# Optimization experiments

Measured on AMD Instinct MI355X. Metric: run time of the kernel, lower is better.

Reference implementation:

```python
import jax, jax.numpy as jnp
import numpy as np

N_NODES = 50000
N_EDGES = 1600000
N_GRAPHS = 512
HEADS = 4
HEAD_DIM = 32
LAYERS = 3
NEG_SLOPE = 0.2


def setup_inputs() -> dict:
    key = jax.random.key(0)
    ks = jax.random.split(key, 7)
    x = jax.random.normal(ks[0], (N_NODES, 128), dtype=jnp.float32)
    Ws = jax.random.normal(ks[1], (LAYERS, 128, 128), dtype=jnp.float32) * 0.1
    att_src = jax.random.normal(ks[2], (LAYERS, HEADS, HEAD_DIM), dtype=jnp.float32) * 0.1
    att_dst = jax.random.normal(ks[3], (LAYERS, HEADS, HEAD_DIM), dtype=jnp.float32) * 0.1
    biases = jnp.zeros((LAYERS, 128), dtype=jnp.float32)
    edge_index = jax.random.randint(ks[4], (2, N_EDGES), 0, N_NODES, dtype=jnp.int64)
    batch = jnp.sort(jax.random.randint(ks[5], (N_NODES,), 0, N_GRAPHS, dtype=jnp.int64))
    return {"x": x, "Ws": Ws, "att_src": att_src, "att_dst": att_dst,
            "biases": biases, "edge_index": edge_index, "batch": batch}


def _gat_layer(x, W, a_s, a_d, b, src, dst, n):
    # linear transform -> per-head features [N, H, C]
    h = (x @ W).reshape(n, HEADS, HEAD_DIM)
    # per-node attention halves [N, H]
    alpha_src = jnp.einsum('nhc,hc->nh', h, a_s)
    alpha_dst = jnp.einsum('nhc,hc->nh', h, a_d)
    # edge logits [E, H]
    e = jax.nn.leaky_relu(alpha_src[src] + alpha_dst[dst], NEG_SLOPE)
    # segment softmax over incoming edges of each destination node
    m = jax.ops.segment_max(e, dst, num_segments=n)
    w = jnp.exp(e - m[dst])
    denom = jax.ops.segment_sum(w, dst, num_segments=n)
    alpha = w / (denom[dst] + 1e-16)
    # weighted scatter-add of source features [E, H, C] -> [N, H, C]
    msg = h[src] * alpha[:, :, None]
    out = jax.ops.segment_sum(msg, dst, num_segments=n)
    return out.reshape(n, HEADS * HEAD_DIM) + b


def reference(x, Ws, att_src, att_dst, biases, edge_index, batch):
    n = x.shape[0]
    # PyG GATConv adds self-loops by default
    loops = jnp.arange(n, dtype=edge_index.dtype)
    src = jnp.concatenate([edge_index[0], loops])
    dst = jnp.concatenate([edge_index[1], loops])
    for l in range(LAYERS):
        x = jax.nn.elu(_gat_layer(x, Ws[l], att_src[l], att_dst[l], biases[l], src, dst, n))
        # dropout is identity in eval mode
    # global mean pool over graphs
    sums = jax.ops.segment_sum(x, batch, num_segments=N_GRAPHS)
    cnt = jax.ops.segment_sum(jnp.ones((n,), x.dtype), batch, num_segments=N_GRAPHS)
    return sums / jnp.maximum(cnt, 1.0)[:, None]
```

## Files before the change

kernel.cpp:

```cpp
#include <hip/hip_runtime.h>
#include <hip/hip_fp16.h>
#include <math.h>

#define HEADS 4
#define HDIM 32
#define FD 128
#define NEG 0.2f
#define BCAP 4608
#define CH 8192
#define CHW 128

typedef _Float16 f16x8 __attribute__((ext_vector_type(8)));
typedef float f32x4 __attribute__((ext_vector_type(4)));

__device__ __forceinline__ float lrelu(float x) { return fmaxf(x, NEG * x); }

__global__ __launch_bounds__(256) void k_prep(const float* __restrict__ x,
                                              __half* __restrict__ o, long nF,
                                              const float* __restrict__ W,
                                              const float* __restrict__ att_s,
                                              const float* __restrict__ att_d,
                                              _Float16* __restrict__ W16T,
                                              float* __restrict__ va_s,
                                              float* __restrict__ va_d,
                                              int* __restrict__ bcnt, int nbuck,
                                              int ncvt) {
    int b = blockIdx.x;
    if (b < ncvt) {
        long i = ((long)b * 256 + threadIdx.x) * 4;
        if (i < nF) {
            float4 v = *(const float4*)&x[i];
            *(__half2*)&o[i] = __floats2half2_rn(v.x, v.y);
            *(__half2*)&o[i + 2] = __floats2half2_rn(v.z, v.w);
        }
        return;
    }
    if (b == ncvt + 3) {
        for (int i = threadIdx.x; i < nbuck; i += 256) bcnt[i] = 0;
        return;
    }
    int l = b - ncvt;
    const float* Wl = W + (long)l * FD * FD;
    _Float16* ow = W16T + (long)l * FD * FD;
    for (int i = threadIdx.x; i < FD * FD; i += 256) {
        int k = i >> 7, n = i & 127;
        ow[n * FD + k] = (_Float16)Wl[i];
    }
    const float* as_l = att_s + l * HEADS * HDIM;
    const float* ad_l = att_d + l * HEADS * HDIM;
    for (int idx = threadIdx.x; idx < HEADS * FD; idx += 256) {
        int hd = idx >> 7, k = idx & 127;
        float ss = 0.f, dd = 0.f;
        for (int c = 0; c < HDIM; ++c) {
            float w = Wl[k * FD + hd * HDIM + c];
            ss += w * as_l[hd * HDIM + c];
            dd += w * ad_l[hd * HDIM + c];
        }
        va_s[(long)l * HEADS * FD + idx] = ss;
        va_d[(long)l * HEADS * FD + idx] = dd;
    }
}

__global__ __launch_bounds__(256) void k_gemm_mfma(const __half* __restrict__ x16,
                                                   const _Float16* __restrict__ W16T,
                                                   __half* __restrict__ h, int N) {
    __shared__ _Float16 wl[FD * FD];
    int t = threadIdx.x;
    for (int i = t * 8; i < FD * FD; i += 2048)
        *(f16x8*)&wl[i] = *(const f16x8*)&W16T[i];

    int w = t >> 6, lane = t & 63;
    int m = lane & 15, quad = lane >> 4;
    int row0 = blockIdx.x * 128 + w * 32;

    f16x8 a[2][4];
    f16x8 zf = {};
#pragma unroll
    for (int rt = 0; rt < 2; ++rt) {
        int gr = row0 + rt * 16 + m;
#pragma unroll
        for (int kc = 0; kc < 4; ++kc)
            a[rt][kc] = (gr < N) ? *(const f16x8*)&x16[(long)gr * FD + kc * 32 + quad * 8] : zf;
    }
    f32x4 acc[2][8];
#pragma unroll
    for (int rt = 0; rt < 2; ++rt)
#pragma unroll
        for (int c = 0; c < 8; ++c) acc[rt][c] = (f32x4){0.f, 0.f, 0.f, 0.f};

    __syncthreads();
#pragma unroll
    for (int c = 0; c < 8; ++c) {
        int nb = c * 16 + m;
#pragma unroll
        for (int kc = 0; kc < 4; ++kc) {
            f16x8 b = *(f16x8*)&wl[nb * FD + kc * 32 + quad * 8];
            acc[0][c] = __builtin_amdgcn_mfma_f32_16x16x32_f16(a[0][kc], b, acc[0][c], 0, 0, 0);
            acc[1][c] = __builtin_amdgcn_mfma_f32_16x16x32_f16(a[1][kc], b, acc[1][c], 0, 0, 0);
        }
    }
#pragma unroll
    for (int rt = 0; rt < 2; ++rt) {
        int rbase = row0 + rt * 16 + quad * 4;
#pragma unroll
        for (int c = 0; c < 8; ++c) {
            int col = c * 16 + m;
#pragma unroll
            for (int i = 0; i < 4; ++i) {
                int gr = rbase + i;
                if (gr < N) h[(long)gr * FD + col] = __float2half(acc[rt][c][i]);
            }
        }
    }
}

__global__ __launch_bounds__(256) void k_alpha(const __half* __restrict__ h,
                                               const float* __restrict__ a_s,
                                               const float* __restrict__ a_d,
                                               float* __restrict__ as_o,
                                               float* __restrict__ ad_o, int N) {
    int t = threadIdx.x;
    int n = blockIdx.x * 16 + (t >> 4);
    if (n >= N) return;
    int c16 = t & 15, gh = c16 >> 2, cb = c16 * 8;
    int c32 = (c16 & 3) * 8;
    float4 raw = *(const float4*)&h[(long)n * FD + cb];
    const __half* hh = (const __half*)&raw;
    float vs = 0.f, vd = 0.f;
#pragma unroll
    for (int i = 0; i < 8; ++i) {
        float hv = __half2float(hh[i]);
        vs += hv * a_s[gh * HDIM + c32 + i];
        vd += hv * a_d[gh * HDIM + c32 + i];
    }
    vs += __shfl_xor(vs, 1); vs += __shfl_xor(vs, 2);
    vd += __shfl_xor(vd, 1); vd += __shfl_xor(vd, 2);
    if ((c16 & 3) == 0) {
        as_o[n * HEADS + gh] = vs;
        ad_o[n * HEADS + gh] = vd;
    }
}

__global__ __launch_bounds__(1024) void k_bin(const int* __restrict__ ei, int NE,
                                              int nbuck,
                                              int* __restrict__ bcnt,
                                              int* __restrict__ binned) {
    __shared__ int hist[512];
    __shared__ int gbase[512];
    int t = threadIdx.x;
    int c0 = blockIdx.x * CH;
    if (t < 512) hist[t] = 0;
    __syncthreads();
    int sub[8], val[8], loff[8];
#pragma unroll
    for (int k = 0; k < 8; ++k) {
        int idx = c0 + k * 1024 + t;
        sub[k] = -1;
        if (idx < NE) {
            int s = ei[idx], d = ei[NE + idx];
            sub[k] = d >> 7;
            val[k] = s | ((d & 127) << 16);
            loff[k] = atomicAdd(&hist[sub[k]], 1);
        }
    }
    __syncthreads();
    if (t < 512 && t < nbuck && hist[t] > 0)
        gbase[t] = atomicAdd(&bcnt[t], hist[t]);
    __syncthreads();
#pragma unroll
    for (int k = 0; k < 8; ++k) {
        if (sub[k] >= 0) {
            int p = gbase[sub[k]] + loff[k];
            if (p < BCAP) binned[(long)sub[k] * BCAP + p] = val[k];
        }
    }
}

__global__ __launch_bounds__(1024) void k_scan_sub(const int* __restrict__ bcnt,
                                                   int* __restrict__ bbase, int n,
                                                   int* __restrict__ rowstart, int N, int NE,
                                                   float* __restrict__ cnt, int G,
                                                   float* __restrict__ outz) {
    __shared__ int sm[1024];
    int t = threadIdx.x;
    int c0 = t * 4;
    int v0 = (c0 < n) ? bcnt[c0] : 0;
    int v1 = (c0 + 1 < n) ? bcnt[c0 + 1] : 0;
    int v2 = (c0 + 2 < n) ? bcnt[c0 + 2] : 0;
    int v3 = (c0 + 3 < n) ? bcnt[c0 + 3] : 0;
    int tot = v0 + v1 + v2 + v3;
    sm[t] = tot;
    if (t < G) cnt[t] = 0.f;
    __syncthreads();
    for (int off = 1; off < 1024; off <<= 1) {
        int u = (t >= off) ? sm[t - off] : 0;
        __syncthreads();
        sm[t] += u;
        __syncthreads();
    }
    int base = sm[t] - tot;
    if (c0 < n) bbase[c0] = base;
    if (c0 + 1 < n) bbase[c0 + 1] = base + v0;
    if (c0 + 2 < n) bbase[c0 + 2] = base + v0 + v1;
    if (c0 + 3 < n) bbase[c0 + 3] = base + v0 + v1 + v2;
    if (t == 1023) {
        bbase[n] = sm[1023];
        rowstart[N] = NE;
    }
    long tot_out = (long)G * FD;
    for (long i = t * 4; i < tot_out; i += 4096)
        *(float4*)&outz[i] = (float4){0.f, 0.f, 0.f, 0.f};
}

__global__ __launch_bounds__(256) void k_bucket_csr(const int* __restrict__ binned,
                                                    const int* __restrict__ bcnt,
                                                    const int* __restrict__ bbase,
                                                    int* __restrict__ csr_src,
                                                    int* __restrict__ rowstart, int N) {
    int b = blockIdx.x;
    int t = threadIdx.x;
    __shared__ int ldeg[128], lofs[128], lcur[128];
    __shared__ int lcsr[BCAP];
    if (t < 128) ldeg[t] = 0;
    __syncthreads();
    int cnt = bcnt[b];
    if (cnt > BCAP) cnt = BCAP;
    int base = bbase[b];
    const int* reg = binned + (long)b * BCAP;
    for (int i = t; i < cnt; i += 256)
        atomicAdd(&ldeg[reg[i] >> 16], 1);
    __syncthreads();
    if (t < 128) lofs[t] = ldeg[t];
    __syncthreads();
    for (int off = 1; off < 128; off <<= 1) {
        int u = (t < 128 && t >= off) ? lofs[t - off] : 0;
        __syncthreads();
        if (t < 128) lofs[t] += u;
        __syncthreads();
    }
    if (t < 128) lcur[t] = lofs[t] - ldeg[t];
    __syncthreads();
    for (int i = t; i < cnt; i += 256) {
        int v = reg[i];
        int p = atomicAdd(&lcur[v >> 16], 1);
        lcsr[p] = v & 0xFFFF;
    }
    __syncthreads();
    for (int i = t; i < cnt; i += 256) csr_src[base + i] = lcsr[i];
    if (t < 128) {
        int d = b * 128 + t;
        if (d < N) rowstart[d] = base + lofs[t] - ldeg[t];
    }
}

__global__ __launch_bounds__(256) void k_aggr(const int* __restrict__ csr_src,
                                              const int* __restrict__ rowstart,
                                              const float* __restrict__ as_,
                                              const float* __restrict__ ad_,
                                              const __half* __restrict__ h,
                                              const float* __restrict__ bias,
                                              const float* __restrict__ va_s,
                                              const float* __restrict__ va_d,
                                              float* __restrict__ as_n,
                                              float* __restrict__ ad_n,
                                              __half* __restrict__ out, int N) {
    __shared__ int s_all[4][CHW];
    __shared__ float w_all[4][CHW * 4];
    int t = threadIdx.x;
    int wv = t >> 6, lane = t & 63;
    int n = blockIdx.x * 4 + wv;
    if (n >= N) return;
    int* s_lds = s_all[wv];
    float* w_lds = w_all[wv];
    int c16 = lane & 15, rg = lane >> 4;
    int gh = c16 >> 2;
    int cb = c16 * 8;
    int we = lane >> 2, hd = lane & 3;
    int beg = rowstart[n], end = rowstart[n + 1];
    int deg = end - beg;
    float adn_w = ad_[n * HEADS + hd];
    float l = 0.f;
    float acc[8] = {0.f, 0.f, 0.f, 0.f, 0.f, 0.f, 0.f, 0.f};

    for (int c0 = 0; c0 < deg; c0 += CHW) {
        int cnt = deg - c0;
        if (cnt > CHW) cnt = CHW;
        for (int i = lane; i < cnt; i += 64) s_lds[i] = csr_src[beg + c0 + i];
        __builtin_amdgcn_wave_barrier();
        for (int e = we; e < cnt; e += 16) {
            int s = s_lds[e];
            float lg = lrelu(as_[s * HEADS + hd] + adn_w);
            float w = __expf(fminf(lg, 30.f));
            w_lds[e * 4 + hd] = w;
            l += w;
        }
        __builtin_amdgcn_wave_barrier();
#pragma unroll 2
        for (int e = rg; e < cnt; e += 4) {
            int s = s_lds[e];
            float w = w_lds[e * 4 + gh];
            float4 raw = *(const float4*)&h[(long)s * FD + cb];
            const __half* hh = (const __half*)&raw;
#pragma unroll
            for (int i = 0; i < 8; ++i)
                acc[i] += __half2float(hh[i]) * w;
        }
        __builtin_amdgcn_wave_barrier();
    }
    l += __shfl_xor(l, 4);
    l += __shfl_xor(l, 8);
    l += __shfl_xor(l, 16);
    l += __shfl_xor(l, 32);
    float l_gh = __shfl(l, gh);
#pragma unroll
    for (int i = 0; i < 8; ++i) {
        acc[i] += __shfl_xor(acc[i], 16);
        acc[i] += __shfl_xor(acc[i], 32);
    }
    float adn_g = ad_[n * HEADS + gh];
    float sl = lrelu(as_[n * HEADS + gh] + adn_g);
    float sw = __expf(fminf(sl, 30.f));
    float inv = 1.f / (l_gh + sw + 1e-16f);
    float4 rawh = *(const float4*)&h[(long)n * FD + cb];
    const __half* hh = (const __half*)&rawh;
    float4 b0 = *(const float4*)&bias[cb];
    float4 b1 = *(const float4*)&bias[cb + 4];
    float bb[8] = {b0.x, b0.y, b0.z, b0.w, b1.x, b1.y, b1.z, b1.w};
    float v[8];
#pragma unroll
    for (int i = 0; i < 8; ++i) {
        float u = (acc[i] + sw * __half2float(hh[i])) * inv + bb[i];
        v[i] = u > 0.f ? u : expm1f(u);
    }
    if (rg == 0) {
        __half o8[8];
#pragma unroll
        for (int i = 0; i < 8; ++i) o8[i] = __float2half(v[i]);
        *(float4*)&out[(long)n * FD + cb] = *(float4*)o8;
    }
    if (va_s) {
        const float* vs = va_s + rg * FD + cb;
        const float* vd = va_d + rg * FD + cb;
        float ps = 0.f, pd = 0.f;
#pragma unroll
        for (int i = 0; i < 8; ++i) {
            ps += v[i] * vs[i];
            pd += v[i] * vd[i];
        }
        for (int off = 1; off < 16; off <<= 1) {
            ps += __shfl_xor(ps, off);
            pd += __shfl_xor(pd, off);
        }
        if (c16 == 0) {
            as_n[n * HEADS + rg] = ps;
            ad_n[n * HEADS + rg] = pd;
        }
    }
}

__global__ __launch_bounds__(128) void k_pool(const __half* __restrict__ x,
                                              const int* __restrict__ batch,
                                              float* __restrict__ out,
                                              float* __restrict__ cnt, int N) {
    int n0 = blockIdx.x * 32;
    if (n0 >= N) return;
    int n1 = n0 + 32;
    if (n1 > N) n1 = N;
    int ch = threadIdx.x;
    __shared__ int gb[32];
    if (ch < n1 - n0) gb[ch] = batch[n0 + ch];
    __syncthreads();
    int g = gb[0];
    float sum = 0.f, c_local = 0.f;
    for (int n = n0; n < n1; ++n) {
        int gn = gb[n - n0];
        if (gn != g) {
            atomicAdd(&out[(long)g * FD + ch], sum);
            if (ch == 0) atomicAdd(&cnt[g], c_local);
            sum = 0.f;
            c_local = 0.f;
            g = gn;
        }
        sum += __half2float(x[(long)n * FD + ch]);
        c_local += 1.f;
    }
    atomicAdd(&out[(long)g * FD + ch], sum);
    if (ch == 0) atomicAdd(&cnt[g], c_local);
}

__global__ void k_div(float* __restrict__ out, const float* __restrict__ cnt, int G) {
    int i = blockIdx.x * 256 + threadIdx.x;
    if (i >= G * FD) return;
    float c = cnt[i >> 7];
    out[i] /= (c > 1.f ? c : 1.f);
}

extern "C" void kernel_launch(void* const* d_in, const int* in_sizes, int n_in,
                              void* d_out, int out_size, void* d_ws, size_t ws_size,
                              hipStream_t stream) {
    const float* x0     = (const float*)d_in[0];
    const float* Wall   = (const float*)d_in[1];
    const float* att_s  = (const float*)d_in[2];
    const float* att_d  = (const float*)d_in[3];
    const float* biases = (const float*)d_in[4];
    const int*   ei     = (const int*)d_in[5];
    const int*   batch  = (const int*)d_in[6];
    float*       out    = (float*)d_out;

    int N  = in_sizes[0] / FD;
    int NE = in_sizes[5] / 2;
    int G  = out_size / FD;

    int nbuck = (N + 127) >> 7;

    long nF = (long)N * FD;
    float*    wsf      = (float*)d_ws;
    float*    asA      = wsf;
    float*    adA      = asA + (long)N * HEADS;
    float*    asB      = adA + (long)N * HEADS;
    float*    adB      = asB + (long)N * HEADS;
    float*    cnt      = adB + (long)N * HEADS;
    float*    va_s     = cnt + G;
    float*    va_d     = va_s + 3 * HEADS * FD;
    int*      rowstart = (int*)(va_d + 3 * HEADS * FD);
    int*      bcnt     = rowstart + N + 1;
    int*      bbase    = bcnt + nbuck;
    int*      csr_src  = bbase + nbuck + 1;
    __half*   h        = (__half*)(csr_src + NE);
    __half*   x16      = h + nF;
    _Float16* W16T     = (_Float16*)(x16 + nF);
    int*      binned   = (int*)(W16T + 3 * FD * FD);

    int ncvt = (int)((nF / 4 + 255) / 256);

    k_prep<<<ncvt + 4, 256, 0, stream>>>(x0, x16, nF, Wall, att_s, att_d,
                                         W16T, va_s, va_d, bcnt, nbuck, ncvt);
    k_bin<<<(NE + CH - 1) / CH, 1024, 0, stream>>>(ei, NE, nbuck, bcnt, binned);
    k_scan_sub<<<1, 1024, 0, stream>>>(bcnt, bbase, nbuck, rowstart, N, NE, cnt, G, out);
    k_bucket_csr<<<nbuck, 256, 0, stream>>>(binned, bcnt, bbase, csr_src, rowstart, N);

    float* asR[3] = {asA, asB, asA};
    float* adR[3] = {adA, adB, adA};
    for (int l = 0; l < 3; ++l) {
        k_gemm_mfma<<<(N + 127) / 128, 256, 0, stream>>>(x16, W16T + (long)l * FD * FD, h, N);
        if (l == 0)
            k_alpha<<<(N + 15) / 16, 256, 0, stream>>>(h, att_s, att_d, asA, adA, N);
        const float* vs = (l < 2) ? va_s + (long)(l + 1) * HEADS * FD : nullptr;
        const float* vd = (l < 2) ? va_d + (long)(l + 1) * HEADS * FD : nullptr;
        k_aggr<<<(N + 3) / 4, 256, 0, stream>>>(csr_src, rowstart, asR[l], adR[l], h,
                                                biases + l * FD, vs, vd,
                                                asR[l + 1 < 3 ? l + 1 : 0],
                                                adR[l + 1 < 3 ? l + 1 : 0], x16, N);
    }

    k_pool<<<(N + 31) / 32, 128, 0, stream>>>(x16, batch, out, cnt, N);
    k_div<<<(G * FD + 255) / 256, 256, 0, stream>>>(out, cnt, G);
}
```

Measured before the change: 371.5 us.

## Fuse attention-weight and feature-gather passes in GAT aggregation kernel

Restructures the per-node aggregation so each lane group of 8 handles one edge at a time: it computes the edge's softmax weight for its own head and immediately gathers 16 half-precision features, instead of writing weights to LDS in one pass and reading them back in a second. This removes the LDS weight buffer, one wave barrier and a second pass over the neighbor indices, and processes 8 edges concurrently rather than 4. In exchange each lane keeps 16 accumulators, which raises register pressure, and the exp/leaky-relu is recomputed redundantly by the two lanes sharing a head.

After: 427.3 us. +15.0%, slower.

```diff
diff --git a/kernel.cpp b/kernel.cpp
--- a/kernel.cpp
+++ b/kernel.cpp
@@ -265,95 +265,99 @@
                                               float* __restrict__ ad_n,
                                               __half* __restrict__ out, int N) {
     __shared__ int s_all[4][CHW];
-    __shared__ float w_all[4][CHW * 4];
     int t = threadIdx.x;
     int wv = t >> 6, lane = t & 63;
     int n = blockIdx.x * 4 + wv;
     if (n >= N) return;
     int* s_lds = s_all[wv];
-    float* w_lds = w_all[wv];
-    int c16 = lane & 15, rg = lane >> 4;
-    int gh = c16 >> 2;
-    int cb = c16 * 8;
-    int we = lane >> 2, hd = lane & 3;
+    int c8 = lane & 7, rg = lane >> 3;
+    int gh = c8 >> 1;
+    int cb = c8 * 16;
     int beg = rowstart[n], end = rowstart[n + 1];
     int deg = end - beg;
-    float adn_w = ad_[n * HEADS + hd];
+    float adn = ad_[n * HEADS + gh];
     float l = 0.f;
-    float acc[8] = {0.f, 0.f, 0.f, 0.f, 0.f, 0.f, 0.f, 0.f};
+    float acc[16];
+#pragma unroll
+    for (int i = 0; i < 16; ++i) acc[i] = 0.f;
 
     for (int c0 = 0; c0 < deg; c0 += CHW) {
         int cnt = deg - c0;
         if (cnt > CHW) cnt = CHW;
         for (int i = lane; i < cnt; i += 64) s_lds[i] = csr_src[beg + c0 + i];
         __builtin_amdgcn_wave_barrier();
-        for (int e = we; e < cnt; e += 16) {
+#pragma unroll 2
+        for (int e = rg; e < cnt; e += 8) {
             int s = s_lds[e];
-            float lg = lrelu(as_[s * HEADS + hd] + adn_w);
+            float lg = lrelu(as_[s * HEADS + gh] + adn);
             float w = __expf(fminf(lg, 30.f));
-            w_lds[e * 4 + hd] = w;
             l += w;
+            const __half* hp = &h[(long)s * FD + cb];
+            float4 r0 = *(const float4*)hp;
+            float4 r1 = *(const float4*)(hp + 8);
+            const __half* h0 = (const __half*)&r0;
+            const __half* h1 = (const __half*)&r1;
+#pragma unroll
+            for (int i = 0; i < 8; ++i) {
+                acc[i] += __half2float(h0[i]) * w;
+                acc[8 + i] += __half2float(h1[i]) * w;
+            }
         }
         __builtin_amdgcn_wave_barrier();
-#pragma unroll 2
-        for (int e = rg; e < cnt; e += 4) {
-            int s = s_lds[e];
-            float w = w_lds[e * 4 + gh];
-            float4 raw = *(const float4*)&h[(long)s * FD + cb];
-            const __half* hh = (const __half*)&raw;
-#pragma unroll
-            for (int i = 0; i < 8; ++i)
-                acc[i] += __half2float(hh[i]) * w;
-        }
-        __builtin_amdgcn_wave_barrier();
-    }
-    l += __shfl_xor(l, 4);
+    }
     l += __shfl_xor(l, 8);
     l += __shfl_xor(l, 16);
     l += __shfl_xor(l, 32);
-    float l_gh = __shfl(l, gh);
-#pragma unroll
-    for (int i = 0; i < 8; ++i) {
+#pragma unroll
+    for (int i = 0; i < 16; ++i) {
+        acc[i] += __shfl_xor(acc[i], 8);
         acc[i] += __shfl_xor(acc[i], 16);
         acc[i] += __shfl_xor(acc[i], 32);
     }
-    float adn_g = ad_[n * HEADS + gh];
-    float sl = lrelu(as_[n * HEADS + gh] + adn_g);
+    float sl = lrelu(as_[n * HEADS + gh] + adn);
     float sw = __expf(fminf(sl, 30.f));
-    float inv = 1.f / (l_gh + sw + 1e-16f);
-    float4 rawh = *(const float4*)&h[(long)n * FD + cb];
-    const __half* hh = (const __half*)&rawh;
+    float inv = 1.f / (l + sw + 1e-16f);
+    const __half* hn = &h[(long)n * FD + cb];
+    float4 rh0 = *(const float4*)hn;
+    float4 rh1 = *(const float4*)(hn + 8);
+    const __half* hh0 = (const __half*)&rh0;
+    const __half* hh1 = (const __half*)&rh1;
     float4 b0 = *(const float4*)&bias[cb];
     float4 b1 = *(const float4*)&bias[cb + 4];
-    float bb[8] = {b0.x, b0.y, b0.z, b0.w, b1.x, b1.y, b1.z, b1.w};
-    float v[8];
+    float4 b2 = *(const float4*)&bias[cb + 8];
+    float4 b3 = *(const float4*)&bias[cb + 12];
+    float bb[16] = {b0.x, b0.y, b0.z, b0.w, b1.x, b1.y, b1.z, b1.w,
+                    b2.x, b2.y, b2.z, b2.w, b3.x, b3.y, b3.z, b3.w};
+    float v[16];
 #pragma unroll
     for (int i = 0; i < 8; ++i) {
-        float u = (acc[i] + sw * __half2float(hh[i])) * inv + bb[i];
-        v[i] = u > 0.f ? u : expm1f(u);
+        float u0 = (acc[i] + sw * __half2float(hh0[i])) * inv + bb[i];
+        v[i] = u0 > 0.f ? u0 : expm1f(u0);
+        float u1 = (acc[8 + i] + sw * __half2float(hh1[i])) * inv + bb[8 + i];
+        v[8 + i] = u1 > 0.f ? u1 : expm1f(u1);
     }
     if (rg == 0) {
-        __half o8[8];
-#pragma unroll
-        for (int i = 0; i < 8; ++i) o8[i] = __float2half(v[i]);
-        *(float4*)&out[(long)n * FD + cb] = *(float4*)o8;
+        __half o16[16];
+#pragma unroll
+        for (int i = 0; i < 16; ++i) o16[i] = __float2half(v[i]);
+        *(float4*)&out[(long)n * FD + cb] = ((float4*)o16)[0];
+        *(float4*)&out[(long)n * FD + cb + 8] = ((float4*)o16)[1];
     }
     if (va_s) {
-        const float* vs = va_s + rg * FD + cb;
-        const float* vd = va_d + rg * FD + cb;
+        int hd = rg & 3;
+        const float* vsp = va_s + hd * FD + cb;
+        const float* vdp = va_d + hd * FD + cb;
         float ps = 0.f, pd = 0.f;
 #pragma unroll
-        for (int i = 0; i < 8; ++i) {
-            ps += v[i] * vs[i];
-            pd += v[i] * vd[i];
-        }
-        for (int off = 1; off < 16; off <<= 1) {
-            ps += __shfl_xor(ps, off);
-            pd += __shfl_xor(pd, off);
-        }
-        if (c16 == 0) {
-            as_n[n * HEADS + rg] = ps;
-            ad_n[n * HEADS + rg] = pd;
+        for (int i = 0; i < 16; ++i) {
+            ps += v[i] * vsp[i];
+            pd += v[i] * vdp[i];
+        }
+        ps += __shfl_xor(ps, 1); ps += __shfl_xor(ps, 2); ps += __shfl_xor(ps, 4);
+        pd += __shfl_xor(pd, 1); pd += __shfl_xor(pd, 2); pd += __shfl_xor(pd, 4);
+        if (c8 == 0 && rg < 4) {
+            as_n[n * HEADS + hd] = ps;
+            ad_n[n * HEADS + hd] = pd;
         }
     }
 }
```

## Precompute per-edge attention weights in a separate fp16 edge kernel

Applied to the files above, without the earlier changes.

Adds a k_edgew kernel per layer that computes the exponentiated leaky-relu attention weight for every CSR edge and all 4 heads, and stores the results as fp16. To make this possible, the CSR build now also writes a 16-bit destination index per edge. k_aggr then reads the weights contiguously instead of gathering source alphas and computing exp in a separate LDS pass, which removes a wave phase and the LDS weight buffer. In exchange it adds a launch per layer and writes and reads an extra NE*8-byte weight array. Storing the weights as fp16 also risks precision loss or overflow for large logits.

Measured after the change: 390.6 us. 1.05x slower.

```diff
diff --git a/kernel.cpp b/kernel.cpp
--- a/kernel.cpp
+++ b/kernel.cpp
@@ -216,6 +216,7 @@
                                                     const int* __restrict__ bcnt,
                                                     const int* __restrict__ bbase,
                                                     int* __restrict__ csr_src,
+                                                    unsigned short* __restrict__ dst16,
                                                     int* __restrict__ rowstart, int N) {
     int b = blockIdx.x;
     int t = threadIdx.x;
@@ -243,18 +244,43 @@
     for (int i = t; i < cnt; i += 256) {
         int v = reg[i];
         int p = atomicAdd(&lcur[v >> 16], 1);
-        lcsr[p] = v & 0xFFFF;
-    }
-    __syncthreads();
-    for (int i = t; i < cnt; i += 256) csr_src[base + i] = lcsr[i];
+        lcsr[p] = v;
+    }
+    __syncthreads();
+    for (int i = t; i < cnt; i += 256) {
+        int v = lcsr[i];
+        csr_src[base + i] = v & 0xFFFF;
+        dst16[base + i] = (unsigned short)(b * 128 + (v >> 16));
+    }
     if (t < 128) {
         int d = b * 128 + t;
         if (d < N) rowstart[d] = base + lofs[t] - ldeg[t];
     }
 }
 
+__global__ __launch_bounds__(256) void k_edgew(const int* __restrict__ csr_src,
+                                               const unsigned short* __restrict__ dst16,
+                                               const float4* __restrict__ as4,
+                                               const float4* __restrict__ ad4,
+                                               __half* __restrict__ alpha, int NE) {
+    int e = blockIdx.x * 256 + threadIdx.x;
+    if (e >= NE) return;
+    int s = csr_src[e];
+    int d = dst16[e];
+    float4 a = as4[s];
+    float4 b = ad4[d];
+    float w0 = __expf(fminf(lrelu(a.x + b.x), 30.f));
+    float w1 = __expf(fminf(lrelu(a.y + b.y), 30.f));
+    float w2 = __expf(fminf(lrelu(a.z + b.z), 30.f));
+    float w3 = __expf(fminf(lrelu(a.w + b.w), 30.f));
+    __half2* o = (__half2*)&alpha[(long)e * 4];
+    o[0] = __floats2half2_rn(w0, w1);
+    o[1] = __floats2half2_rn(w2, w3);
+}
+
 __global__ __launch_bounds__(256) void k_aggr(const int* __restrict__ csr_src,
                                               const int* __restrict__ rowstart,
+                                              const __half* __restrict__ alpha,
                                               const float* __restrict__ as_,
                                               const float* __restrict__ ad_,
                                               const __half* __restrict__ h,
@@ -265,20 +291,16 @@
                                               float* __restrict__ ad_n,
                                               __half* __restrict__ out, int N) {
     __shared__ int s_all[4][CHW];
-    __shared__ float w_all[4][CHW * 4];
     int t = threadIdx.x;
     int wv = t >> 6, lane = t & 63;
     int n = blockIdx.x * 4 + wv;
     if (n >= N) return;
     int* s_lds = s_all[wv];
-    float* w_lds = w_all[wv];
     int c16 = lane & 15, rg = lane >> 4;
     int gh = c16 >> 2;
     int cb = c16 * 8;
-    int we = lane >> 2, hd = lane & 3;
     int beg = rowstart[n], end = rowstart[n + 1];
     int deg = end - beg;
-    float adn_w = ad_[n * HEADS + hd];
     float l = 0.f;
     float acc[8] = {0.f, 0.f, 0.f, 0.f, 0.f, 0.f, 0.f, 0.f};
 
@@ -286,19 +308,13 @@
         int cnt = deg - c0;
         if (cnt > CHW) cnt = CHW;
         for (int i = lane; i < cnt; i += 64) s_lds[i] = csr_src[beg + c0 + i];
-        __builtin_amdgcn_wave_barrier();
-        for (int e = we; e < cnt; e += 16) {
-            int s = s_lds[e];
-            float lg = lrelu(as_[s * HEADS + hd] + adn_w);
-            float w = __expf(fminf(lg, 30.f));
-            w_lds[e * 4 + hd] = w;
-            l += w;
-        }
+        const __half* ap = alpha + (long)(beg + c0) * 4;
         __builtin_amdgcn_wave_barrier();
 #pragma unroll 2
         for (int e = rg; e < cnt; e += 4) {
             int s = s_lds[e];
-            float w = w_lds[e * 4 + gh];
+            float w = __half2float(ap[e * 4 + gh]);
+            l += w;
             float4 raw = *(const float4*)&h[(long)s * FD + cb];
             const __half* hh = (const __half*)&raw;
 #pragma unroll
@@ -307,20 +323,17 @@
         }
         __builtin_amdgcn_wave_barrier();
     }
-    l += __shfl_xor(l, 4);
-    l += __shfl_xor(l, 8);
     l += __shfl_xor(l, 16);
     l += __shfl_xor(l, 32);
-    float l_gh = __shfl(l, gh);
 #pragma unroll
     for (int i = 0; i < 8; ++i) {
         acc[i] += __shfl_xor(acc[i], 16);
         acc[i] += __shfl_xor(acc[i], 32);
     }
-    float adn_g = ad_[n * HEADS + gh];
-    float sl = lrelu(as_[n * HEADS + gh] + adn_g);
+    float adn = ad_[n * HEADS + gh];
+    float sl = lrelu(as_[n * HEADS + gh] + adn);
     float sw = __expf(fminf(sl, 30.f));
-    float inv = 1.f / (l_gh + sw + 1e-16f);
+    float inv = 1.f / (l + sw + 1e-16f);
     float4 rawh = *(const float4*)&h[(long)n * FD + cb];
     const __half* hh = (const __half*)&rawh;
     float4 b0 = *(const float4*)&bias[cb];
@@ -426,10 +439,12 @@
     int*      bcnt     = rowstart + N + 1;
     int*      bbase    = bcnt + nbuck;
     int*      csr_src  = bbase + nbuck + 1;
-    __half*   h        = (__half*)(csr_src + NE);
+    unsigned short* dst16 = (unsigned short*)(csr_src + NE);
+    __half*   h        = (__half*)(dst16 + ((NE + 1) & ~1));
     __half*   x16      = h + nF;
     _Float16* W16T     = (_Float16*)(x16 + nF);
-    int*      binned   = (int*)(W16T + 3 * FD * FD);
+    __half*   alpha    = (__half*)(W16T + 3 * FD * FD);
+    int*      binned   = (int*)(alpha + (long)NE * 4);
 
     int ncvt = (int)((nF / 4 + 255) / 256);
 
@@ -437,7 +452,7 @@
                                          W16T, va_s, va_d, bcnt, nbuck, ncvt);
     k_bin<<<(NE + CH - 1) / CH, 1024, 0, stream>>>(ei, NE, nbuck, bcnt, binned);
     k_scan_sub<<<1, 1024, 0, stream>>>(bcnt, bbase, nbuck, rowstart, N, NE, cnt, G, out);
-    k_bucket_csr<<<nbuck, 256, 0, stream>>>(binned, bcnt, bbase, csr_src, rowstart, N);
+    k_bucket_csr<<<nbuck, 256, 0, stream>>>(binned, bcnt, bbase, csr_src, dst16, rowstart, N);
 
     float* asR[3] = {asA, asB, asA};
     float* adR[3] = {adA, adB, adA};
@@ -445,9 +460,12 @@
         k_gemm_mfma<<<(N + 127) / 128, 256, 0, stream>>>(x16, W16T + (long)l * FD * FD, h, N);
         if (l == 0)
             k_alpha<<<(N + 15) / 16, 256, 0, stream>>>(h, att_s, att_d, asA, adA, N);
+        k_edgew<<<(NE + 255) / 256, 256, 0, stream>>>(csr_src, dst16,
+                                                      (const float4*)asR[l],
+                                                      (const float4*)adR[l], alpha, NE);
         const float* vs = (l < 2) ? va_s + (long)(l + 1) * HEADS * FD : nullptr;
         const float* vd = (l < 2) ? va_d + (long)(l + 1) * HEADS * FD : nullptr;
-        k_aggr<<<(N + 3) / 4, 256, 0, stream>>>(csr_src, rowstart, asR[l], adR[l], h,
+        k_aggr<<<(N + 3) / 4, 256, 0, stream>>>(csr_src, rowstart, alpha, asR[l], adR[l], h,
                                                 biases + l * FD, vs, vd,
                                                 asR[l + 1 < 3 ? l + 1 : 0],
                                                 adR[l + 1 < 3 ? l + 1 : 0], x16, N);
```
